# Optimization experiments

Hardware: AMD Instinct MI355X
Metric: run time of the kernel (lower is better)

The kernel has to match this reference:

```python
import jax, jax.numpy as jnp
import numpy as np

B, L, D = 4, 4096, 2048
DF = 4 * D
CAPACITY_RATIO = 0.5


def setup_inputs() -> dict:
    key = jax.random.key(0)
    ks = jax.random.split(key, 4)
    s = 0.02
    return {
        "x": jax.random.normal(ks[0], (B, L, D), dtype=jnp.float32),
        "w_r": jax.random.normal(ks[1], (D,), dtype=jnp.float32) * s,
        "b_r": jnp.zeros((), dtype=jnp.float32),
        "w1": jax.random.normal(ks[2], (D, DF), dtype=jnp.float32) * s,
        "b1": jnp.zeros((DF,), dtype=jnp.float32),
        "w2": jax.random.normal(ks[3], (DF, D), dtype=jnp.float32) * s,
        "b2": jnp.zeros((D,), dtype=jnp.float32),
    }


def reference(x, w_r, b_r, w1, b1, w2, b2):
    # MoD eval path: router scores -> top-k token indices -> gather ->
    # block (FFN) on selected tokens -> scatter back into zeros.
    b, l, d = x.shape
    k = int(l * CAPACITY_RATIO)
    scores = jnp.einsum("bld,d->bl", x, w_r) + b_r          # [B, L]
    _, idx = jax.lax.top_k(scores, k)                        # [B, k] int32
    x_sel = jnp.take_along_axis(x, idx[:, :, None], axis=1)  # [B, k, D]
    h = jax.nn.gelu(jnp.einsum("bkd,df->bkf", x_sel, w1) + b1)
    out_sel = jnp.einsum("bkf,fd->bkd", h, w2) + b2          # [B, k, D]
    batch_ix = jnp.arange(b)[:, None]                        # [B, 1]
    out = jnp.zeros_like(x).at[batch_ix, idx].set(out_sel)
    return out
```

## Files before the change

kernel.cpp:

```cpp
#include <hip/hip_runtime.h>

#define BB 4
#define LL 4096
#define DD 2048
#define DFF 8192
#define KSEL 2048
#define MROWS (BB * KSEL)

typedef __bf16 bf16x8 __attribute__((ext_vector_type(8)));
typedef float f32x4 __attribute__((ext_vector_type(4)));
typedef unsigned short u16x8 __attribute__((ext_vector_type(8)));

__device__ __forceinline__ unsigned short f2bf(float f) {
    union { float f; unsigned int u; } v; v.f = f;
    unsigned int u = v.u;
    unsigned int r = u + 0x7fffu + ((u >> 16) & 1u);
    return (unsigned short)(r >> 16);
}

__device__ __forceinline__ void gl2lds16(const void* g, void* l) {
    __builtin_amdgcn_global_load_lds(
        (const __attribute__((address_space(1))) void*)g,
        (__attribute__((address_space(3))) void*)l,
        16, 0, 0);
}

__global__ __launch_bounds__(256) void router_conv_kernel(
    const float* __restrict__ x, const float* __restrict__ wr,
    const float* __restrict__ br, float* __restrict__ scores,
    unsigned short* __restrict__ xbf)
{
    const int lane = threadIdx.x & 63;
    const int wave = threadIdx.x >> 6;
    const int tok = blockIdx.x * 4 + wave;
    const float* row = x + (long)tok * DD;
    unsigned short* orow = xbf + (long)tok * DD;
    double acc = 0.0;
#pragma unroll
    for (int it = 0; it < 4; ++it) {
        const int off = it * 512 + lane * 8;
        float4 xv = *(const float4*)(row + off);
        float4 xw = *(const float4*)(row + off + 4);
        float4 wv = *(const float4*)(wr + off);
        float4 ww = *(const float4*)(wr + off + 4);
        acc += (double)xv.x * wv.x + (double)xv.y * wv.y
             + (double)xv.z * wv.z + (double)xv.w * wv.w;
        acc += (double)xw.x * ww.x + (double)xw.y * ww.y
             + (double)xw.z * ww.z + (double)xw.w * ww.w;
        u16x8 o;
        o[0] = f2bf(xv.x); o[1] = f2bf(xv.y); o[2] = f2bf(xv.z); o[3] = f2bf(xv.w);
        o[4] = f2bf(xw.x); o[5] = f2bf(xw.y); o[6] = f2bf(xw.z); o[7] = f2bf(xw.w);
        *(u16x8*)(orow + off) = o;
    }
#pragma unroll
    for (int o = 32; o > 0; o >>= 1) acc += __shfl_down(acc, o);
    if (lane == 0) scores[tok] = (float)(acc + (double)br[0]);
}

__global__ __launch_bounds__(256) void rank_select_kernel(
    const float* __restrict__ scores, int* __restrict__ idxout,
    int* __restrict__ zidxout)
{
    __shared__ float s[LL];
    const int b = blockIdx.y;
    const float* sb = scores + b * LL;
    for (int i = threadIdx.x; i < LL; i += 256) s[i] = sb[i];
    __syncthreads();
    const int t = blockIdx.x * 256 + threadIdx.x;
    const float my = s[t];
    int rank = 0;
#pragma unroll 16
    for (int j = 0; j < LL; ++j) {
        float sj = s[j];
        rank += (sj > my) || (sj == my && j < t);
    }
    if (rank < KSEL) idxout[(b << 11) + rank] = t;
    else             zidxout[(b << 11) + rank - KSEL] = t;
}

__global__ __launch_bounds__(256) void zero_rows_kernel(
    const int* __restrict__ zidx, float* __restrict__ Out)
{
    const int m = blockIdx.x;
    const int b = m >> 11;
    const int tok = zidx[m];
    float* dst = Out + ((long)b * LL + tok) * DD;
    const int c = threadIdx.x * 8;
    float4 z = {0.f, 0.f, 0.f, 0.f};
    *(float4*)(dst + c) = z;
    *(float4*)(dst + c + 4) = z;
}

__global__ __launch_bounds__(256) void conv_transpose2_kernel(
    const float* __restrict__ W1, unsigned short* __restrict__ W1t,
    const float* __restrict__ W2, unsigned short* __restrict__ W2t)
{
    __shared__ unsigned short t[64 * 72];
    int bid = blockIdx.x;
    const float* W; unsigned short* Wt; int KR, NC, bx, by;
    if (bid < 4096) { W = W1; Wt = W1t; KR = DD; NC = DFF; bx = bid & 127; by = bid >> 7; }
    else { bid -= 4096; W = W2; Wt = W2t; KR = DFF; NC = DD; bx = bid & 31; by = bid >> 5; }
    const int n0 = bx * 64;
    const int k0 = by * 64;
    const int tid = threadIdx.x;
    const int rk = tid >> 4;
    const int cn = (tid & 15) * 4;
#pragma unroll
    for (int p = 0; p < 4; ++p) {
        const int k = rk + p * 16;
        float4 v = *(const float4*)(W + (long)(k0 + k) * NC + n0 + cn);
        t[(cn + 0) * 72 + k] = f2bf(v.x);
        t[(cn + 1) * 72 + k] = f2bf(v.y);
        t[(cn + 2) * 72 + k] = f2bf(v.z);
        t[(cn + 3) * 72 + k] = f2bf(v.w);
    }
    __syncthreads();
    const int rn = tid >> 3;
    const int ck = (tid & 7) * 8;
#pragma unroll
    for (int p = 0; p < 2; ++p) {
        const int n = rn + p * 32;
        u16x8 o = *(const u16x8*)&t[n * 72 + ck];
        *(u16x8*)(Wt + (long)(n0 + n) * KR + k0 + ck) = o;
    }
}

#define VM6 asm volatile("s_waitcnt vmcnt(6)" ::: "memory")
#define VM4 asm volatile("s_waitcnt vmcnt(4)" ::: "memory")
#define VM0 asm volatile("s_waitcnt vmcnt(0)" ::: "memory")
#define NOSTG ((void)0)
#define NOVM ((void)0)
#define CFENCE asm volatile("" ::: "memory")

#define STAGE_A(BUF, q, kt) gl2lds16(ga[q] + (kt), &BUF[(q) * 4096 + wave * 512])
#define STAGE_B(BUF, q, kt) gl2lds16(gb[q] + (kt), &BUF[(q) * 4096 + wave * 512])

#define PH0(ABUF, BBUF, STG, VMW) do {                                        \
    const char* ab_ = (const char*)ABUF + aoff;                               \
    const char* bb_ = (const char*)BBUF + boff;                               \
    bf16x8 af_[4];                                                            \
    _Pragma("unroll") for (int i_ = 0; i_ < 4; ++i_)                          \
        af_[i_] = *(const bf16x8*)(ab_ + i_ * 1024);                          \
    _Pragma("unroll") for (int j_ = 0; j_ < 4; ++j_)                          \
        bfr[j_] = *(const bf16x8*)(bb_ + j_ * 1024);                          \
    STG;                                                                      \
    VMW;                                                                      \
    CFENCE; __builtin_amdgcn_s_barrier(); CFENCE;                             \
    __builtin_amdgcn_s_setprio(1);                                            \
    _Pragma("unroll") for (int i_ = 0; i_ < 4; ++i_)                          \
        _Pragma("unroll") for (int j_ = 0; j_ < 4; ++j_)                      \
            acc[i_][j_] = __builtin_amdgcn_mfma_f32_16x16x32_bf16(            \
                af_[i_], bfr[j_], acc[i_][j_], 0, 0, 0);                      \
    __builtin_amdgcn_s_setprio(0);                                            \
    CFENCE; __builtin_amdgcn_s_barrier(); CFENCE;                             \
} while (0)

#define PH1(ABUF, STG, VMW) do {                                              \
    const char* ab_ = (const char*)ABUF + aoff + 4096;                        \
    bf16x8 af_[4];                                                            \
    _Pragma("unroll") for (int i_ = 0; i_ < 4; ++i_)                          \
        af_[i_] = *(const bf16x8*)(ab_ + i_ * 1024);                          \
    STG;                                                                      \
    VMW;                                                                      \
    CFENCE; __builtin_amdgcn_s_barrier(); CFENCE;                             \
    __builtin_amdgcn_s_setprio(1);                                            \
    _Pragma("unroll") for (int i_ = 0; i_ < 4; ++i_)                          \
        _Pragma("unroll") for (int j_ = 0; j_ < 4; ++j_)                      \
            acc[4 + i_][j_] = __builtin_amdgcn_mfma_f32_16x16x32_bf16(        \
                af_[i_], bfr[j_], acc[4 + i_][j_], 0, 0, 0);                  \
    __builtin_amdgcn_s_setprio(0);                                            \
    CFENCE; __builtin_amdgcn_s_barrier(); CFENCE;                             \
} while (0)

template <int MODE, int IND>
__global__ __launch_bounds__(512, 2) void gemm_pipe_kernel(
    const unsigned short* __restrict__ A,
    const unsigned short* __restrict__ Bt,
    const float* __restrict__ bias,
    unsigned short* __restrict__ H,
    const int* __restrict__ idx,
    float* __restrict__ Out,
    int K, int N)
{
    __shared__ unsigned short As0[8192], As1[8192], As2[8192], As3[8192];
    __shared__ unsigned short Bs0[8192], Bs1[8192], Bs2[8192], Bs3[8192];
    const int tid = threadIdx.x;
    const int lane = tid & 63;
    const int wave = tid >> 6;
    const int wm = wave >> 2;
    const int wn = wave & 3;

    const int NN = N >> 8;
    const int nwg = (int)gridDim.x;
    const int per = nwg >> 3;
    const int wg = ((int)blockIdx.x & 7) * per + ((int)blockIdx.x >> 3);
    const int gsz = 4 * NN;
    const int gidx = wg / gsz;
    const int rem = wg - gidx * gsz;
    const int pm = gidx * 4 + (rem & 3);
    const int pn = rem >> 2;
    const long m0 = (long)pm * 256;
    const long n0 = (long)pn * 256;

    const int cr = tid >> 2;
    const int cl = (tid & 3) ^ ((cr >> 1) & 3);
    const unsigned short* ga[2];
    const unsigned short* gb[2];
#pragma unroll
    for (int q = 0; q < 2; ++q) {
        const int r = q * 128 + cr;
        long ar;
        if constexpr (IND) {
            const int sel = (int)m0 + r;
            ar = (long)(sel >> 11) * LL + idx[sel];
        } else {
            ar = m0 + r;
        }
        ga[q] = A + ar * (long)K + cl * 8;
        gb[q] = Bt + (n0 + r) * (long)K + cl * 8;
    }

    const int l15 = lane & 15;
    const int lg = lane >> 4;
    const int ko = ((lg ^ ((l15 >> 1) & 3)) << 4);
    const int aoff = (wm * 128 + l15) * 64 + ko;
    const int boff = (wn * 64 + l15) * 64 + ko;

    f32x4 acc[8][4];
#pragma unroll
    for (int i = 0; i < 8; ++i)
#pragma unroll
        for (int j = 0; j < 4; ++j) {
            f32x4 z = {0.f, 0.f, 0.f, 0.f};
            acc[i][j] = z;
        }
    bf16x8 bfr[4];

    const int NT = K >> 5;

    STAGE_A(As0, 0, 0);  STAGE_A(As0, 1, 0);
    STAGE_B(Bs0, 0, 0);  STAGE_B(Bs0, 1, 0);
    STAGE_A(As1, 0, 32); STAGE_A(As1, 1, 32);
    STAGE_B(Bs1, 0, 32); STAGE_B(Bs1, 1, 32);
    STAGE_A(As2, 0, 64); STAGE_A(As2, 1, 64);
    VM6;
    CFENCE; __builtin_amdgcn_s_barrier(); CFENCE;

    int kb = 64, ka = 96;
    for (int it = 0; it < (NT - 4) / 4; ++it) {
        PH0(As0, Bs0, (STAGE_B(Bs2, 0, kb), STAGE_B(Bs2, 1, kb)), NOVM);
        PH1(As0,      (STAGE_A(As3, 0, ka), STAGE_A(As3, 1, ka)), VM6);
        kb += 32; ka += 32;
        PH0(As1, Bs1, (STAGE_B(Bs3, 0, kb), STAGE_B(Bs3, 1, kb)), NOVM);
        PH1(As1,      (STAGE_A(As0, 0, ka), STAGE_A(As0, 1, ka)), VM6);
        kb += 32; ka += 32;
        PH0(As2, Bs2, (STAGE_B(Bs0, 0, kb), STAGE_B(Bs0, 1, kb)), NOVM);
        PH1(As2,      (STAGE_A(As1, 0, ka), STAGE_A(As1, 1, ka)), VM6);
        kb += 32; ka += 32;
        PH0(As3, Bs3, (STAGE_B(Bs1, 0, kb), STAGE_B(Bs1, 1, kb)), NOVM);
        PH1(As3,      (STAGE_A(As2, 0, ka), STAGE_A(As2, 1, ka)), VM6);
        kb += 32; ka += 32;
    }
    PH0(As0, Bs0, (STAGE_B(Bs2, 0, kb), STAGE_B(Bs2, 1, kb)), NOVM);
    PH1(As0,      (STAGE_A(As3, 0, ka), STAGE_A(As3, 1, ka)), VM6);
    kb += 32;
    PH0(As1, Bs1, (STAGE_B(Bs3, 0, kb), STAGE_B(Bs3, 1, kb)), NOVM);
    PH1(As1, NOSTG, VM4);
    PH0(As2, Bs2, NOSTG, NOVM);
    PH1(As2, NOSTG, VM0);
    PH0(As3, Bs3, NOSTG, NOVM);
    PH1(As3, NOSTG, NOVM);

    if constexpr (MODE == 0) {
        const long rowb = m0 + wm * 128 + (lg << 2);
        const int colb = (int)n0 + wn * 64 + l15;
#pragma unroll
        for (int i = 0; i < 8; ++i) {
#pragma unroll
            for (int j = 0; j < 4; ++j) {
                const int col = colb + j * 16;
                const float bv = bias[col];
#pragma unroll
                for (int r = 0; r < 4; ++r) {
                    const long row = rowb + i * 16 + r;
                    float v = acc[i][j][r] + bv;
                    float u = v + 0.044715f * v * v * v;
                    float e = __expf(1.5957691216057308f * u);
                    float g = v - v * __builtin_amdgcn_rcpf(1.0f + e);
                    H[row * N + col] = f2bf(g);
                }
            }
        }
    } else {
        const int rowb = (int)m0 + wm * 128 + (lg << 2);
        const int colb = (int)n0 + wn * 64 + l15;
#pragma unroll
        for (int i = 0; i < 8; ++i) {
            int ob[4];
#pragma unroll
            for (int r = 0; r < 4; ++r) {
                const int row = rowb + i * 16 + r;
                const int b = row >> 11;
                const int tok = idx[(b << 11) + (row & (KSEL - 1))];
                ob[r] = (b * LL + tok) * DD;
            }
#pragma unroll
            for (int j = 0; j < 4; ++j) {
                const int col = colb + j * 16;
                const float bv = bias[col];
#pragma unroll
                for (int r = 0; r < 4; ++r)
                    Out[(long)ob[r] + col] = acc[i][j][r] + bv;
            }
        }
    }
}

extern "C" void kernel_launch(void* const* d_in, const int* in_sizes, int n_in,
                              void* d_out, int out_size, void* d_ws, size_t ws_size,
                              hipStream_t stream)
{
    const float* x  = (const float*)d_in[0];
    const float* wr = (const float*)d_in[1];
    const float* br = (const float*)d_in[2];
    const float* w1 = (const float*)d_in[3];
    const float* b1 = (const float*)d_in[4];
    const float* w2 = (const float*)d_in[5];
    const float* b2 = (const float*)d_in[6];
    float* out = (float*)d_out;

    char* ws = (char*)d_ws;
    float* scores = (float*)ws;              ws += (long)BB * LL * 4;
    int* idx  = (int*)ws;                    ws += (long)BB * KSEL * 4;
    int* zidx = (int*)ws;                    ws += (long)BB * (LL - KSEL) * 4;
    unsigned short* xbf  = (unsigned short*)ws; ws += (long)BB * LL * DD * 2;
    unsigned short* w1t  = (unsigned short*)ws; ws += (long)DFF * DD * 2;
    unsigned short* w2t  = (unsigned short*)ws; ws += (long)DD * DFF * 2;
    unsigned short* h    = (unsigned short*)ws; ws += (long)MROWS * DFF * 2;

    router_conv_kernel<<<(BB * LL) / 4, 256, 0, stream>>>(x, wr, br, scores, xbf);
    conv_transpose2_kernel<<<8192, 256, 0, stream>>>(w1, w1t, w2, w2t);
    rank_select_kernel<<<dim3(LL / 256, BB), 256, 0, stream>>>(scores, idx, zidx);
    zero_rows_kernel<<<BB * (LL - KSEL), 256, 0, stream>>>(zidx, out);
    gemm_pipe_kernel<0, 1><<<(MROWS / 256) * (DFF / 256), 512, 0, stream>>>(
        xbf, w1t, b1, h, idx, nullptr, DD, DFF);
    gemm_pipe_kernel<1, 0><<<(MROWS / 256) * (DD / 256), 512, 0, stream>>>(
        h, w2t, b2, nullptr, idx, out, DFF, DD);
}
```

Before: 1.007 ms.

## Merge split GEMM half-phases into one tile step with a single barrier

Replaces the two half-phases (PH0/PH1), each with two barriers, by one TILE step per 32-wide k-slice. Each step does one vmcnt wait and one barrier up front, loads both A halves and B from LDS, then issues all 32 MFMAs. A and B staging now happen together, three tiles ahead, in the 4-buffer ring. This cuts barrier count and synchronisation stalls per k-step. In exchange it holds more fragment registers live and loses the finer interleaving of staging with compute.

```diff
diff --git a/kernel.cpp b/kernel.cpp
--- a/kernel.cpp
+++ b/kernel.cpp
@@ -125,51 +125,40 @@
     }
 }
 
-#define VM6 asm volatile("s_waitcnt vmcnt(6)" ::: "memory")
+#define VM8 asm volatile("s_waitcnt vmcnt(8)" ::: "memory")
 #define VM4 asm volatile("s_waitcnt vmcnt(4)" ::: "memory")
 #define VM0 asm volatile("s_waitcnt vmcnt(0)" ::: "memory")
 #define NOSTG ((void)0)
-#define NOVM ((void)0)
 #define CFENCE asm volatile("" ::: "memory")
 
 #define STAGE_A(BUF, q, kt) gl2lds16(ga[q] + (kt), &BUF[(q) * 4096 + wave * 512])
 #define STAGE_B(BUF, q, kt) gl2lds16(gb[q] + (kt), &BUF[(q) * 4096 + wave * 512])
-
-#define PH0(ABUF, BBUF, STG, VMW) do {                                        \
+#define STAGE_AB(AB, BBF, kt) \
+    (STAGE_A(AB, 0, kt), STAGE_A(AB, 1, kt), STAGE_B(BBF, 0, kt), STAGE_B(BBF, 1, kt))
+
+#define TILE(ABUF, BBUF, STG, VMW) do {                                       \
+    VMW;                                                                      \
+    CFENCE; __builtin_amdgcn_s_barrier(); CFENCE;                             \
     const char* ab_ = (const char*)ABUF + aoff;                               \
     const char* bb_ = (const char*)BBUF + boff;                               \
-    bf16x8 af_[4];                                                            \
+    bf16x8 a0_[4], a1_[4];                                                    \
     _Pragma("unroll") for (int i_ = 0; i_ < 4; ++i_)                          \
-        af_[i_] = *(const bf16x8*)(ab_ + i_ * 1024);                          \
+        a0_[i_] = *(const bf16x8*)(ab_ + i_ * 1024);                          \
     _Pragma("unroll") for (int j_ = 0; j_ < 4; ++j_)                          \
         bfr[j_] = *(const bf16x8*)(bb_ + j_ * 1024);                          \
     STG;                                                                      \
-    VMW;                                                                      \
-    CFENCE; __builtin_amdgcn_s_barrier(); CFENCE;                             \
+    _Pragma("unroll") for (int i_ = 0; i_ < 4; ++i_)                          \
+        a1_[i_] = *(const bf16x8*)(ab_ + 4096 + i_ * 1024);                   \
     __builtin_amdgcn_s_setprio(1);                                            \
     _Pragma("unroll") for (int i_ = 0; i_ < 4; ++i_)                          \
         _Pragma("unroll") for (int j_ = 0; j_ < 4; ++j_)                      \
             acc[i_][j_] = __builtin_amdgcn_mfma_f32_16x16x32_bf16(            \
-                af_[i_], bfr[j_], acc[i_][j_], 0, 0, 0);                      \
-    __builtin_amdgcn_s_setprio(0);                                            \
-    CFENCE; __builtin_amdgcn_s_barrier(); CFENCE;                             \
-} while (0)
-
-#define PH1(ABUF, STG, VMW) do {                                              \
-    const char* ab_ = (const char*)ABUF + aoff + 4096;                        \
-    bf16x8 af_[4];                                                            \
-    _Pragma("unroll") for (int i_ = 0; i_ < 4; ++i_)                          \
-        af_[i_] = *(const bf16x8*)(ab_ + i_ * 1024);                          \
-    STG;                                                                      \
-    VMW;                                                                      \
-    CFENCE; __builtin_amdgcn_s_barrier(); CFENCE;                             \
-    __builtin_amdgcn_s_setprio(1);                                            \
+                a0_[i_], bfr[j_], acc[i_][j_], 0, 0, 0);                      \
     _Pragma("unroll") for (int i_ = 0; i_ < 4; ++i_)                          \
         _Pragma("unroll") for (int j_ = 0; j_ < 4; ++j_)                      \
             acc[4 + i_][j_] = __builtin_amdgcn_mfma_f32_16x16x32_bf16(        \
-                af_[i_], bfr[j_], acc[4 + i_][j_], 0, 0, 0);                  \
+                a1_[i_], bfr[j_], acc[4 + i_][j_], 0, 0, 0);                  \
     __builtin_amdgcn_s_setprio(0);                                            \
-    CFENCE; __builtin_amdgcn_s_barrier(); CFENCE;                             \
 } while (0)
 
 template <int MODE, int IND>
@@ -238,38 +227,21 @@
 
     const int NT = K >> 5;
 
-    STAGE_A(As0, 0, 0);  STAGE_A(As0, 1, 0);
-    STAGE_B(Bs0, 0, 0);  STAGE_B(Bs0, 1, 0);
-    STAGE_A(As1, 0, 32); STAGE_A(As1, 1, 32);
-    STAGE_B(Bs1, 0, 32); STAGE_B(Bs1, 1, 32);
-    STAGE_A(As2, 0, 64); STAGE_A(As2, 1, 64);
-    VM6;
-    CFENCE; __builtin_amdgcn_s_barrier(); CFENCE;
-
-    int kb = 64, ka = 96;
+    STAGE_AB(As0, Bs0, 0);
+    STAGE_AB(As1, Bs1, 32);
+    STAGE_AB(As2, Bs2, 64);
+
+    int kk = 96;
     for (int it = 0; it < (NT - 4) / 4; ++it) {
-        PH0(As0, Bs0, (STAGE_B(Bs2, 0, kb), STAGE_B(Bs2, 1, kb)), NOVM);
-        PH1(As0,      (STAGE_A(As3, 0, ka), STAGE_A(As3, 1, ka)), VM6);
-        kb += 32; ka += 32;
-        PH0(As1, Bs1, (STAGE_B(Bs3, 0, kb), STAGE_B(Bs3, 1, kb)), NOVM);
-        PH1(As1,      (STAGE_A(As0, 0, ka), STAGE_A(As0, 1, ka)), VM6);
-        kb += 32; ka += 32;
-        PH0(As2, Bs2, (STAGE_B(Bs0, 0, kb), STAGE_B(Bs0, 1, kb)), NOVM);
-        PH1(As2,      (STAGE_A(As1, 0, ka), STAGE_A(As1, 1, ka)), VM6);
-        kb += 32; ka += 32;
-        PH0(As3, Bs3, (STAGE_B(Bs1, 0, kb), STAGE_B(Bs1, 1, kb)), NOVM);
-        PH1(As3,      (STAGE_A(As2, 0, ka), STAGE_A(As2, 1, ka)), VM6);
-        kb += 32; ka += 32;
-    }
-    PH0(As0, Bs0, (STAGE_B(Bs2, 0, kb), STAGE_B(Bs2, 1, kb)), NOVM);
-    PH1(As0,      (STAGE_A(As3, 0, ka), STAGE_A(As3, 1, ka)), VM6);
-    kb += 32;
-    PH0(As1, Bs1, (STAGE_B(Bs3, 0, kb), STAGE_B(Bs3, 1, kb)), NOVM);
-    PH1(As1, NOSTG, VM4);
-    PH0(As2, Bs2, NOSTG, NOVM);
-    PH1(As2, NOSTG, VM0);
-    PH0(As3, Bs3, NOSTG, NOVM);
-    PH1(As3, NOSTG, NOVM);
+        TILE(As0, Bs0, STAGE_AB(As3, Bs3, kk), VM8); kk += 32;
+        TILE(As1, Bs1, STAGE_AB(As0, Bs0, kk), VM8); kk += 32;
+        TILE(As2, Bs2, STAGE_AB(As1, Bs1, kk), VM8); kk += 32;
+        TILE(As3, Bs3, STAGE_AB(As2, Bs2, kk), VM8); kk += 32;
+    }
+    TILE(As0, Bs0, STAGE_AB(As3, Bs3, kk), VM8);
+    TILE(As1, Bs1, NOSTG, VM8);
+    TILE(As2, Bs2, NOSTG, VM4);
+    TILE(As3, Bs3, NOSTG, VM0);
 
     if constexpr (MODE == 0) {
         const long rowb = m0 + wm * 128 + (lg << 2);
```

Measured after the change: 964.0 us. 4.3% less time.
